# Kernel optimization log

Hardware: AMD Instinct MI355X
Metric: run time of the kernel (lower is better)

The kernel has to match this reference:

```python
import jax, jax.numpy as jnp
import numpy as np

SIG = 512                                   # sigSize
NA = 45                                     # numAngles
SQRT2 = float(np.sqrt(2.0))
DIAG = int(np.ceil(SQRT2 * SIG))            # 725, padded (circle=False) size
PAD = int(np.ceil(SQRT2 * SIG - SIG))       # 213
PAD_BEFORE = (SIG + PAD) // 2 - SIG // 2    # 106
THETA = jnp.asarray(np.deg2rad(np.linspace(0.0, 180.0, NA, endpoint=False)), dtype=jnp.float32)


def _rotate_all(img):
    """Bilinear grid_sample rotation (align_corners=True, zero padding) for all angles.
    img: (B, D, D) -> (B, A, D, D)."""
    D = img.shape[-1]
    c = jnp.linspace(-1.0, 1.0, D, dtype=img.dtype)
    xg = c[None, None, :]                    # column coord j
    yg = c[None, :, None]                    # row coord i
    ct = jnp.cos(THETA)[:, None, None]
    st = jnp.sin(THETA)[:, None, None]
    # affine_grid with R = [[c, s, 0], [-s, c, 0]]
    xs = ct * xg + st * yg                   # (A, D, D)
    ys = -st * xg + ct * yg
    px = (xs + 1.0) * 0.5 * (D - 1)
    py = (ys + 1.0) * 0.5 * (D - 1)
    x0 = jnp.floor(px)
    y0 = jnp.floor(py)
    wx = px - x0
    wy = py - y0
    x0i = x0.astype(jnp.int32)
    y0i = y0.astype(jnp.int32)

    def tap(xi, yi, w):
        valid = (xi >= 0) & (xi < D) & (yi >= 0) & (yi < D)
        xi = jnp.clip(xi, 0, D - 1)
        yi = jnp.clip(yi, 0, D - 1)
        return img[:, yi, xi] * (w * valid)[None]

    return (tap(x0i, y0i, (1 - wx) * (1 - wy)) + tap(x0i + 1, y0i, wx * (1 - wy))
            + tap(x0i, y0i + 1, (1 - wx) * wy) + tap(x0i + 1, y0i + 1, wx * wy))


def radon(x):
    """fmult: x (B,1,S,S) -> sinogram (B,1,D,A), circle=False."""
    xp = jnp.pad(x[:, 0], ((0, 0), (PAD_BEFORE, PAD - PAD_BEFORE), (PAD_BEFORE, PAD - PAD_BEFORE)))
    rot = _rotate_all(xp)                    # (B, A, D, D)
    sino = rot.sum(axis=2)                   # ray-sum over rows -> (B, A, D)
    return jnp.transpose(sino, (0, 2, 1))[:, None]   # (B, 1, D, A)


def iradon(sino):
    """ftran: unfiltered backprojection. sino (B,1,D,A) -> (B,1,S,S)."""
    B, _, D, A = sino.shape
    c = jnp.linspace(-1.0, 1.0, D, dtype=sino.dtype)
    ct = jnp.cos(THETA)[:, None, None]
    st = jnp.sin(THETA)[:, None, None]
    t = ct * c[None, None, :] - st * c[None, :, None]     # (A, D, D) detector coord
    pt = (t + 1.0) * 0.5 * (D - 1)
    t0 = jnp.floor(pt)
    wt = pt - t0
    t0i = t0.astype(jnp.int32)
    s = jnp.transpose(sino[:, 0], (0, 2, 1))               # (B, A, D)

    def tap(ti, w):
        valid = (ti >= 0) & (ti < D)
        tic = jnp.clip(ti, 0, D - 1)
        v = jnp.take_along_axis(s, tic.reshape(1, A, D * D), axis=2).reshape(B, A, D, D)
        return v * (w * valid)[None]

    acc = tap(t0i, 1.0 - wt) + tap(t0i + 1, wt)
    reco = acc.sum(axis=1)                                 # sum over angles
    reco = reco[:, PAD_BEFORE:PAD_BEFORE + SIG, PAD_BEFORE:PAD_BEFORE + SIG]
    return (reco * (jnp.pi / (2.0 * A)))[:, None]


def setup_inputs() -> dict:
    key = jax.random.key(0)
    k1, k2 = jax.random.split(key)
    x = jax.random.normal(k1, (2, 1, SIG, SIG), dtype=jnp.float32)
    y = jax.random.normal(k2, (2, 1, DIAG, NA), dtype=jnp.float32)
    return {"x": x, "y": y}


def reference(x, y):
    # CTClass.grad: per-sample ftran(fmult(x_i) - y_i), vectorized over batch
    return iradon(radon(x) - y)
```

## Files before the change

### kernel.cpp

```cpp
#include <hip/hip_runtime.h>
#include <math.h>

#define SIG 512
#define NA 45
#define DD 725
#define PB 106
#define HALFF 362.0f
#define PI_D 3.14159265358979323846

#define TD2 32
#define TY2 32
#define NT2 23
#define NC42 13
#define RW2 52
#define RH2 47
#define NREG2 640
#define NTILES2 (2 * NA * NT2 * NT2)
#define TGRP (NT2 * NT2)

#define ZSTR 728
#define ZELEMS (2 * NA * ZSTR)
#define TBLOFF ZELEMS
#define DESCOFF 65616
#define DESCI 12
#define BMOFF (DESCOFF + NTILES2 * DESCI)
#define BMWORDS 1492
#define WS_NEED ((BMOFF + BMWORDS) * 4)
#define WS_TBL ((TBLOFF + 2 * NA) * 4)

#define NZB 256
#define NSB 186

#define SEGW2 32

__device__ __forceinline__ float cidx(int i) {
    return -1.0f + (float)i * (2.0f / 724.0f);
}

__device__ __forceinline__ void ref_trig(int a, float& ct, float& st) {
    float thf = (float)((double)(4 * a) * PI_D / 180.0);
    ct = (float)cos((double)thf);
    st = (float)sin((double)thf);
}

__device__ __forceinline__ bool tile_geom(
    int a, int b, int td, int ty, float ct, float st,
    int& dlohi, int& gcb, int& grb, int& nrows, int& kske, int& y0i,
    int& zbase, int& boff, float& pxbase, float& pybase) {
    float X0 = HALFF * (1.0f - ct - st);
    float Y0 = HALFF * (1.0f + st - ct);
    int d0 = td * TD2, dmax = min(d0 + TD2 - 1, DD - 1);
    int y0 = ty * TY2, ymax = min(y0 + TY2 - 1, DD - 1);
    const float lo = (float)(PB - 1), hi = (float)(PB + SIG);

    float Ax0 = fmaf(ct, (float)d0, X0), Ax1 = fmaf(ct, (float)dmax, X0);
    float Axlo = fminf(Ax0, Ax1), Axhi = fmaxf(Ax0, Ax1);
    float Ay0 = fmaf(-st, (float)d0, Y0), Ay1 = fmaf(-st, (float)dmax, Y0);
    float Aylo = fminf(Ay0, Ay1), Ayhi = fmaxf(Ay0, Ay1);
    float ylo = (float)y0, yhi = (float)ymax;
    if (st > 1e-6f) {
        ylo = fmaxf(ylo, (lo - Axhi) / st - 1.0f);
        yhi = fminf(yhi, (hi - Axlo) / st + 1.0f);
    } else if (Axhi <= lo || Axlo >= hi) { return false; }
    if (ct > 1e-6f) {
        ylo = fmaxf(ylo, (lo - Ayhi) / ct - 1.0f);
        yhi = fminf(yhi, (hi - Aylo) / ct + 1.0f);
    } else if (ct < -1e-6f) {
        ylo = fmaxf(ylo, (hi - Aylo) / ct - 1.0f);
        yhi = fminf(yhi, (lo - Ayhi) / ct + 1.0f);
    } else if (Ayhi <= lo || Aylo >= hi) { return false; }
    int yclo = max(y0, (int)ceilf(ylo));
    int ychi = min(ymax, (int)floorf(yhi));
    if (ychi < yclo) return false;
    float yclof = (float)yclo, ychif = (float)ychi;

    float dloF = (float)d0, dhiF = (float)dmax;
    if (ct > 1e-6f) {
        dloF = fmaxf(dloF, (lo - st * ychif - X0) / ct - 1.0f);
        dhiF = fminf(dhiF, (hi - st * yclof - X0) / ct + 1.0f);
    } else if (ct < -1e-6f) {
        dloF = fmaxf(dloF, (hi - st * yclof - X0) / ct - 1.0f);
        dhiF = fminf(dhiF, (lo - st * ychif - X0) / ct + 1.0f);
    }
    if (st > 1e-6f) {
        float yl2 = (ct >= 0.0f) ? yclof : ychif;
        float yh2 = (ct >= 0.0f) ? ychif : yclof;
        dloF = fmaxf(dloF, (Y0 + ct * yl2 - hi) / st - 1.0f);
        dhiF = fminf(dhiF, (Y0 + ct * yh2 - lo) / st + 1.0f);
    }
    int dclo = max(d0, (int)ceilf(dloF));
    int dchi = min(dmax, (int)floorf(dhiF));
    if (dchi < dclo) return false;

    float pxmin = 1e30f, pxmax = -1e30f, pymin = 1e30f, pymax = -1e30f;
    for (int ci = 0; ci < 4; ++ci) {
        float df = (float)((ci & 1) ? dchi : dclo);
        float yf = (float)((ci & 2) ? ychi : yclo);
        float px = fmaf(st, yf, fmaf(ct, df, X0));
        float py = fmaf(ct, yf, fmaf(-st, df, Y0));
        pxmin = fminf(pxmin, px); pxmax = fmaxf(pxmax, px);
        pymin = fminf(pymin, py); pymax = fmaxf(pymax, py);
    }
    int cx0 = (int)floorf(pxmin) - 1;
    int cx1 = (int)floorf(pxmax) + 2;
    int ry0 = (int)floorf(pymin) - 1;
    int ry1 = (int)floorf(pymax) + 2;
    if (cx1 < PB || cx0 >= PB + SIG || ry1 < PB || ry0 >= PB + SIG) return false;

    int cx0a = PB + (((cx0 - PB) >> 2) << 2);
    nrows = min(ry1 - ry0 + 1, RH2);
    gcb = cx0a - PB;
    grb = ry0 - PB;
    dlohi = (dclo - d0) | ((dchi - d0) << 8);
    kske = (yclo - y0) | ((ychi - y0) << 8);
    y0i = y0;
    zbase = (b * NA + a) * ZSTR + 1 + d0;
    boff = b * SIG * SIG;
    pxbase = fmaf(ct, (float)d0, X0) - (float)cx0a;
    pybase = fmaf(-st, (float)d0, Y0) - (float)ry0;
    return true;
}

template <int MODE>
__global__ void prep(const float* __restrict__ yin, float* __restrict__ z,
                     float* __restrict__ tbl, float* __restrict__ zpage,
                     int* __restrict__ desc, unsigned* __restrict__ bmap) {
    __shared__ float s_trig[4];
    __shared__ int s_ag[2];
    if (blockIdx.x < NZB) {
        int i = blockIdx.x * blockDim.x + threadIdx.x;
        if (i < 256) zpage[i] = 0.0f;
        if (MODE >= 1 && blockIdx.x == 0 && threadIdx.x < NA) {
            float ct, st;
            ref_trig(threadIdx.x, ct, st);
            tbl[2 * threadIdx.x] = ct;
            tbl[2 * threadIdx.x + 1] = st;
        }
        if (i >= ZELEMS) return;
        int r = i / ZSTR;
        int c = i - r * ZSTR;
        float v = 0.0f;
        if (c >= 1 && c <= DD) {
            int d = c - 1;
            int a = r % NA;
            int b = r / NA;
            v = -yin[(b * DD + d) * NA + a];
        }
        z[i] = v;
        return;
    }
    if (MODE < 2) return;
    int base = (blockIdx.x - NZB) * blockDim.x;
    if (threadIdx.x < 2) {
        int tl = min(base + (int)threadIdx.x * 255, NTILES2 - 1);
        int ag = tl / TGRP;
        s_ag[threadIdx.x] = ag;
        float ct, st;
        ref_trig(ag % NA, ct, st);
        s_trig[2 * threadIdx.x] = ct;
        s_trig[2 * threadIdx.x + 1] = st;
    }
    __syncthreads();
    int tile = base + threadIdx.x;
    bool live = false;
    int dlohi, gcb, grb, nrows, kske, y0i, zbase, boff;
    float pxbase, pybase;
    float ct = 0.0f, st = 0.0f;
    if (tile < NTILES2) {
        int td = tile % NT2; int rest = tile / NT2;
        int ty = rest % NT2;
        int ag = rest / NT2;
        int a = ag % NA;
        int b = ag / NA;
        int sel = (ag == s_ag[0]) ? 0 : 2;
        ct = s_trig[sel]; st = s_trig[sel + 1];
        live = tile_geom(a, b, td, ty, ct, st, dlohi, gcb, grb, nrows, kske,
                         y0i, zbase, boff, pxbase, pybase);
    }
    unsigned long long m = __ballot(live);
    if ((threadIdx.x & 63) == 0) {
        int w = tile >> 5;
        bmap[w] = (unsigned)m;
        bmap[w + 1] = (unsigned)(m >> 32);
    }
    if (!live) return;
    {
        int nch = (nrows * NC42 + 63) >> 6;
        int rmax = (nch * 64 - 1) / NC42;
        if (grb >= 0 && grb + rmax < SIG && gcb >= 0 && gcb + 52 <= SIG)
            dlohi |= (1 << 16);
    }
    int* dp = desc + tile * DESCI;
    float* fp = (float*)dp;
    dp[0] = dlohi; dp[1] = gcb; dp[2] = grb; dp[3] = nrows;
    dp[4] = kske; fp[5] = pxbase; fp[6] = pybase;
    dp[7] = y0i; dp[8] = zbase; dp[9] = boff;
    fp[10] = ct; fp[11] = st;
}

__device__ __forceinline__ void process_tile32(
    const float* __restrict__ img, const float* __restrict__ zpage,
    float ct, float st,
    int dlohi, int gcb, int grb, int nrows, int kske, int y0i, int zbase,
    float pxbase, float pybase,
    float4* reg4, float* __restrict__ z) {
    float* reg = (float*)reg4;
    int lane = threadIdx.x;

    int nch = (nrows * NC42 + 63) >> 6;
    if (dlohi & (1 << 16)) {
        int r0 = (lane * 5) >> 6;
        int c0 = lane - r0 * NC42;
        const float* src = img + ((grb + r0) << 9) + gcb + (c0 << 2);
        for (int ch = 0; ch < nch; ++ch) {
            __builtin_amdgcn_global_load_lds(
                (const __attribute__((address_space(1))) void*)src,
                (__attribute__((address_space(3))) void*)(reg4 + (ch << 6)),
                16, 0, 0);
            bool cy = (c0 != 0);
            src += cy ? (5 * SIG - 4) : (4 * SIG + 48);
            c0 = cy ? (c0 - 1) : (NC42 - 1);
        }
    } else {
        for (int ch = 0; ch < nch; ++ch) {
            int vi = (ch << 6) + lane;
            int r = vi / NC42;
            int c = vi - r * NC42;
            int gr = grb + r;
            int gc = gcb + (c << 2);
            bool valid = ((unsigned)gr < SIG) & ((unsigned)gc < SIG);
            const float* src = valid ? (img + (gr << 9) + gc) : zpage;
            __builtin_amdgcn_global_load_lds(
                (const __attribute__((address_space(1))) void*)src,
                (__attribute__((address_space(3))) void*)(reg4 + (ch << 6)),
                16, 0, 0);
        }
    }
    __syncthreads();

    int half = lane >> 5;
    int dl = lane & 31;
    int ksb = kske & 255, keb = kske >> 8;
    int dlo = dlohi & 255, dhi = (dlohi >> 8) & 255;
    int n = keb - ksb + 1;
    int sq = ksb + ((n * half) >> 1);
    int eq = ksb + ((n * (half + 1)) >> 1) - 1;

    float lf = (float)min(max(dl, dlo), dhi);
    float pxd = fmaf(ct, lf, pxbase);
    float pyd = fmaf(-st, lf, pybase);
    float yif = (float)(y0i + sq);
    float px = fmaf(st, yif, pxd);
    float py = fmaf(ct, yif, pyd);
    float sum = 0.0f;
#pragma unroll 4
    for (int k = sq; k <= eq; ++k) {
        float fx = floorf(px), fy = floorf(py);
        float wx = px - fx, wy = py - fy;
        int addr = (int)fmaf(fy, (float)RW2, fx);
        float v00 = reg[addr],       v10 = reg[addr + 1];
        float v01 = reg[addr + RW2], v11 = reg[addr + RW2 + 1];
        float top = fmaf(wx, v10 - v00, v00);
        float bot = fmaf(wx, v11 - v01, v01);
        sum = fmaf(wy, bot - top, sum + top);
        px += st; py += ct;
    }
    sum += __shfl_xor(sum, 32);
    if (half == 0 && dl >= dlo && dl <= dhi) {
        atomicAdd(&z[zbase + dl], sum);
    }
}

__global__ __launch_bounds__(64) void radon32f(const float* __restrict__ x,
                                               const float* __restrict__ zpage,
                                               const int* __restrict__ desc,
                                               const unsigned* __restrict__ bmap,
                                               float* __restrict__ z) {
    __shared__ float4 reg4[NREG2];
    unsigned w = bmap[blockIdx.x >> 5];
    if (!((w >> (blockIdx.x & 31)) & 1u)) return;
    const int* dp = desc + blockIdx.x * DESCI;
    const float* fp = (const float*)dp;
    process_tile32(x + dp[9], zpage, fp[10], fp[11],
                   dp[0], dp[1], dp[2], dp[3], dp[4], dp[7], dp[8],
                   fp[5], fp[6], reg4, z);
}

template <int TBL>
__global__ __launch_bounds__(64) void radon32(const float* __restrict__ x,
                                              const float* __restrict__ zpage,
                                              const float* __restrict__ tbl,
                                              float* __restrict__ z) {
    __shared__ float4 reg4[NREG2];
    int tile = blockIdx.x;
    int td = tile % NT2; int rest = tile / NT2;
    int ty = rest % NT2; rest /= NT2;
    int a = rest % NA;
    int b = rest / NA;
    float ct, st;
    if (TBL) { ct = tbl[2 * a]; st = tbl[2 * a + 1]; }
    else     { ref_trig(a, ct, st); }
    int dlohi, gcb, grb, nrows, kske, y0i, zbase, boff;
    float pxbase, pybase;
    if (!tile_geom(a, b, td, ty, ct, st, dlohi, gcb, grb, nrows, kske, y0i,
                   zbase, boff, pxbase, pybase)) return;
    process_tile32(x + boff, zpage, ct, st, dlohi, gcb, grb, nrows, kske,
                   y0i, zbase, pxbase, pybase, reg4, z);
}

template <int TBL>
__global__ __launch_bounds__(256) void iradon16(const float* __restrict__ z,
                                                const float* __restrict__ tbl,
                                                float* __restrict__ out) {
    __shared__ float s_sc[NA], s_st2[NA];
    __shared__ int s_lo[NA];
    __shared__ float s_B[NA * 16];
    __shared__ float s_seg[NA * SEGW2];

    int t = threadIdx.x;
    int b = blockIdx.x >> 10;
    int tb = blockIdx.x & 1023;
    int i0 = (tb >> 5) << 4;
    int j0 = (tb & 31) << 4;

    if (t < NA) {
        float ct, st;
        if (TBL) { ct = tbl[2 * t]; st = tbl[2 * t + 1]; }
        else     { ref_trig(t, ct, st); }
        float sc = ct * HALFF;
        float st2 = -st * HALFF;
        float cxl = cidx(j0 + PB), cxh = cidx(j0 + 15 + PB);
        float cyl = cidx(i0 + PB), cyh = cidx(i0 + 15 + PB);
        float a00 = fmaf(sc, cxl, fmaf(st2, cyl, 363.0f));
        float a01 = fmaf(sc, cxl, fmaf(st2, cyh, 363.0f));
        float a10 = fmaf(sc, cxh, fmaf(st2, cyl, 363.0f));
        float a11 = fmaf(sc, cxh, fmaf(st2, cyh, 363.0f));
        float mn = fminf(fminf(a00, a01), fminf(a10, a11));
        int lo = (int)floorf(mn) - 1;
        lo = min(max(lo, 0), ZSTR - 1 - SEGW2);
        s_sc[t] = sc; s_st2[t] = st2; s_lo[t] = lo;
    }
    __syncthreads();

    for (int s = t; s < NA * 16; s += 256) {
        int a = s >> 4, ii = s & 15;
        s_B[s] = fmaf(s_st2[a], cidx(i0 + ii + PB), 363.0f - (float)s_lo[a]);
    }
    const float* zb = z + b * NA * ZSTR;
    for (int s = t; s < NA * SEGW2; s += 256) {
        int a = s >> 5, idx = s & 31;
        s_seg[s] = zb[a * ZSTR + s_lo[a] + idx];
    }
    __syncthreads();

    float cxv = cidx(j0 + (t & 15) + PB);
    int r0 = t >> 4;
    float acc = 0.f;
    for (int a = 0; a < NA; ++a) {
        float af = fmaf(s_sc[a], cxv, s_B[(a << 4) + r0]);
        float fl = floorf(af);
        float wt = af - fl;
        int ia = (int)fl;
        const float* sp = s_seg + (a << 5) + ia;
        float v0 = sp[0], v1 = sp[1];
        acc = fmaf(wt, v1 - v0, acc + v0);
    }
    const float sfin = (float)(PI_D / (2.0 * NA));
    out[(b << 18) + ((i0 + r0) << 9) + j0 + (t & 15)] = acc * sfin;
}

extern "C" void kernel_launch(void* const* d_in, const int* in_sizes, int n_in,
                              void* d_out, int out_size, void* d_ws, size_t ws_size,
                              hipStream_t stream) {
    const float* x = (const float*)d_in[0];
    const float* yin = (const float*)d_in[1];
    float* out = (float*)d_out;
    float* z = (float*)d_ws;
    float* tbl = z + TBLOFF;
    int* desc = (int*)(z + DESCOFF);
    unsigned* bmap = (unsigned*)(z + BMOFF);
    float* zpage = out;

    if (ws_size >= (size_t)WS_NEED) {
        prep<2><<<NZB + NSB, 256, 0, stream>>>(yin, z, tbl, zpage, desc, bmap);
        radon32f<<<NTILES2, 64, 0, stream>>>(x, zpage, desc, bmap, z);
        iradon16<1><<<2048, 256, 0, stream>>>(z, tbl, out);
    } else if (ws_size >= (size_t)WS_TBL) {
        prep<1><<<NZB, 256, 0, stream>>>(yin, z, tbl, zpage, nullptr, nullptr);
        radon32<1><<<NTILES2, 64, 0, stream>>>(x, zpage, tbl, z);
        iradon16<1><<<2048, 256, 0, stream>>>(z, tbl, out);
    } else {
        prep<0><<<NZB, 256, 0, stream>>>(yin, z, nullptr, zpage, nullptr, nullptr);
        radon32<0><<<NTILES2, 64, 0, stream>>>(x, zpage, nullptr, z);
        iradon16<0><<<2048, 256, 0, stream>>>(z, nullptr, out);
    }
}
```

Baseline: 40.45 us.

## Replace tiled radon with strip blocks writing two half-planes, drop prep and atomics

The radon stage now launches one 64-thread block per (batch, angle, detector column tile, half), looping over 32-row chunks of its half of the ray. Each block writes its partial sums plus half the negated measurement straight into one of two z planes, with no atomics. The backprojection sums the two planes while it loads. This removes the prep kernel, the descriptor/bitmap pass and the atomic adds, cutting three launches to two. In exchange there are far fewer radon blocks (4140 vs ~47k), each looping serially over many rows, which lowers parallelism and may leave long-running blocks.

```diff
diff --git a/kernel.cpp b/kernel.cpp
--- a/kernel.cpp
+++ b/kernel.cpp
@@ -9,28 +9,20 @@
 #define PI_D 3.14159265358979323846
 
 #define TD2 32
-#define TY2 32
 #define NT2 23
 #define NC42 13
 #define RW2 52
 #define RH2 47
 #define NREG2 640
+#define NSTRIP (2 * NA * NT2 * 2)
 #define NTILES2 (2 * NA * NT2 * NT2)
-#define TGRP (NT2 * NT2)
 
 #define ZSTR 728
-#define ZELEMS (2 * NA * ZSTR)
-#define TBLOFF ZELEMS
-#define DESCOFF 65616
-#define DESCI 12
-#define BMOFF (DESCOFF + NTILES2 * DESCI)
-#define BMWORDS 1492
-#define WS_NEED ((BMOFF + BMWORDS) * 4)
-#define WS_TBL ((TBLOFF + 2 * NA) * 4)
+#define ZPLANE (2 * NA * ZSTR)
+#define WS_NEED (2 * ZPLANE * 4)
+#define WS_FB (ZPLANE * 4)
 
 #define NZB 256
-#define NSB 186
-
 #define SEGW2 32
 
 __device__ __forceinline__ float cidx(int i) {
@@ -43,16 +35,266 @@
     st = (float)sin((double)thf);
 }
 
-__device__ __forceinline__ bool tile_geom(
-    int a, int b, int td, int ty, float ct, float st,
-    int& dlohi, int& gcb, int& grb, int& nrows, int& kske, int& y0i,
-    int& zbase, int& boff, float& pxbase, float& pybase) {
+__global__ __launch_bounds__(64) void radon_strip(
+    const float* __restrict__ x, const float* __restrict__ yin,
+    float* __restrict__ z01) {
+    __shared__ float4 reg4[NREG2];
+    float* reg = (float*)reg4;
+    int lane = threadIdx.x;
+
+    int bid = blockIdx.x;
+    int h = bid & 1; bid >>= 1;
+    int td = bid % NT2; bid /= NT2;
+    int a = bid % NA;
+    int b = bid / NA;
+
+    float ct, st;
+    ref_trig(a, ct, st);
     float X0 = HALFF * (1.0f - ct - st);
     float Y0 = HALFF * (1.0f + st - ct);
     int d0 = td * TD2, dmax = min(d0 + TD2 - 1, DD - 1);
-    int y0 = ty * TY2, ymax = min(y0 + TY2 - 1, DD - 1);
     const float lo = (float)(PB - 1), hi = (float)(PB + SIG);
 
+    float Ax0 = fmaf(ct, (float)d0, X0), Ax1 = fmaf(ct, (float)dmax, X0);
+    float Axlo = fminf(Ax0, Ax1), Axhi = fmaxf(Ax0, Ax1);
+    float Ay0 = fmaf(-st, (float)d0, Y0), Ay1 = fmaf(-st, (float)dmax, Y0);
+    float Aylo = fminf(Ay0, Ay1), Ayhi = fmaxf(Ay0, Ay1);
+    float ylo = 0.0f, yhi = (float)(DD - 1);
+    bool dead = false;
+    if (st > 1e-6f) {
+        ylo = fmaxf(ylo, (lo - Axhi) / st - 1.0f);
+        yhi = fminf(yhi, (hi - Axlo) / st + 1.0f);
+    } else if (Axhi <= lo || Axlo >= hi) { dead = true; }
+    if (ct > 1e-6f) {
+        ylo = fmaxf(ylo, (lo - Ayhi) / ct - 1.0f);
+        yhi = fminf(yhi, (hi - Aylo) / ct + 1.0f);
+    } else if (ct < -1e-6f) {
+        ylo = fmaxf(ylo, (hi - Aylo) / ct - 1.0f);
+        yhi = fminf(yhi, (lo - Ayhi) / ct + 1.0f);
+    } else if (Ayhi <= lo || Aylo >= hi) { dead = true; }
+    int yclo = max(0, (int)ceilf(ylo));
+    int ychi = min(DD - 1, (int)floorf(yhi));
+    int hs = 0, he = -1;
+    if (!dead && ychi >= yclo) {
+        int n = ychi - yclo + 1;
+        hs = yclo + ((n * h) >> 1);
+        he = yclo + ((n * (h + 1)) >> 1) - 1;
+    }
+
+    int dl = lane & 31;
+    int half = lane >> 5;
+    int dAbs = d0 + dl;
+    float acc = 0.0f;
+
+    for (int k0 = hs; k0 <= he; k0 += 32) {
+        int k1 = min(k0 + 31, he);
+        float k0f = (float)k0, k1f = (float)k1;
+        float dloF = (float)d0, dhiF = (float)dmax;
+        if (ct > 1e-6f) {
+            dloF = fmaxf(dloF, (lo - st * k1f - X0) / ct - 1.0f);
+            dhiF = fminf(dhiF, (hi - st * k0f - X0) / ct + 1.0f);
+        } else if (ct < -1e-6f) {
+            dloF = fmaxf(dloF, (hi - st * k0f - X0) / ct - 1.0f);
+            dhiF = fminf(dhiF, (lo - st * k1f - X0) / ct + 1.0f);
+        }
+        if (st > 1e-6f) {
+            float yl2 = (ct >= 0.0f) ? k0f : k1f;
+            float yh2 = (ct >= 0.0f) ? k1f : k0f;
+            dloF = fmaxf(dloF, (Y0 + ct * yl2 - hi) / st - 1.0f);
+            dhiF = fminf(dhiF, (Y0 + ct * yh2 - lo) / st + 1.0f);
+        }
+        int dclo = max(d0, (int)ceilf(dloF));
+        int dchi = min(dmax, (int)floorf(dhiF));
+        if (dchi < dclo) continue;
+
+        float pxmin = 1e30f, pxmax = -1e30f, pymin = 1e30f, pymax = -1e30f;
+        for (int ci = 0; ci < 4; ++ci) {
+            float df = (float)((ci & 1) ? dchi : dclo);
+            float yf = (ci & 2) ? k1f : k0f;
+            float px_ = fmaf(st, yf, fmaf(ct, df, X0));
+            float py_ = fmaf(ct, yf, fmaf(-st, df, Y0));
+            pxmin = fminf(pxmin, px_); pxmax = fmaxf(pxmax, px_);
+            pymin = fminf(pymin, py_); pymax = fmaxf(pymax, py_);
+        }
+        int cx0 = (int)floorf(pxmin) - 1;
+        int ry0 = (int)floorf(pymin) - 1;
+        int ry1 = (int)floorf(pymax) + 2;
+        int cx0a = PB + (((cx0 - PB) >> 2) << 2);
+        int gcb = cx0a - PB;
+        int grb = ry0 - PB;
+        int nrows = min(ry1 - ry0 + 1, RH2);
+        int nch = (nrows * NC42 + 63) >> 6;
+
+        __syncthreads();
+
+        if ((grb >= 0) & (grb + 49 < SIG) & (gcb >= 0) & (gcb + 52 <= SIG)) {
+            int r0 = (lane * 5) >> 6;
+            int c0 = lane - r0 * NC42;
+            const float* src = x + (b << 18) + ((grb + r0) << 9) + gcb + (c0 << 2);
+            for (int ch = 0; ch < nch; ++ch) {
+                __builtin_amdgcn_global_load_lds(
+                    (const __attribute__((address_space(1))) void*)src,
+                    (__attribute__((address_space(3))) void*)(reg4 + (ch << 6)),
+                    16, 0, 0);
+                bool cy = (c0 != 0);
+                src += cy ? (5 * SIG - 4) : (4 * SIG + 48);
+                c0 = cy ? (c0 - 1) : (NC42 - 1);
+            }
+        } else {
+            float4 zv = {0.0f, 0.0f, 0.0f, 0.0f};
+            for (int i = lane; i < (nch << 6); i += 64) reg4[i] = zv;
+            asm volatile("s_waitcnt lgkmcnt(0)" ::: "memory");
+            for (int ch = 0; ch < nch; ++ch) {
+                int vi = (ch << 6) + lane;
+                int r = vi / NC42;
+                int c = vi - r * NC42;
+                int gr = grb + r;
+                int gc = gcb + (c << 2);
+                if (((unsigned)gr < SIG) & ((unsigned)gc < SIG)) {
+                    const float* src = x + (b << 18) + (gr << 9) + gc;
+                    __builtin_amdgcn_global_load_lds(
+                        (const __attribute__((address_space(1))) void*)src,
+                        (__attribute__((address_space(3))) void*)(reg4 + (ch << 6)),
+                        16, 0, 0);
+                }
+            }
+        }
+        __syncthreads();
+
+        int wn = k1 - k0 + 1;
+        int sq = k0 + ((wn * half) >> 1);
+        int eq = k0 + ((wn * (half + 1)) >> 1) - 1;
+        float lf = (float)min(max(dAbs, dclo), dchi);
+        float pxb = X0 - (float)cx0a;
+        float pyb = Y0 - (float)ry0;
+        float px = fmaf(st, (float)sq, fmaf(ct, lf, pxb));
+        float py = fmaf(ct, (float)sq, fmaf(-st, lf, pyb));
+        float psum = 0.0f;
+#pragma unroll 4
+        for (int k = sq; k <= eq; ++k) {
+            float fx = floorf(px), fy = floorf(py);
+            float wx = px - fx, wy = py - fy;
+            int addr = (int)fmaf(fy, (float)RW2, fx);
+            float v00 = reg[addr],       v10 = reg[addr + 1];
+            float v01 = reg[addr + RW2], v11 = reg[addr + RW2 + 1];
+            float top = fmaf(wx, v10 - v00, v00);
+            float bot = fmaf(wx, v11 - v01, v01);
+            psum = fmaf(wy, bot - top, psum + top);
+            px += st; py += ct;
+        }
+        acc += (dAbs >= dclo && dAbs <= dchi) ? psum : 0.0f;
+    }
+
+    acc += __shfl_xor(acc, 32);
+    if (half == 0 && dAbs < DD) {
+        float yv = yin[(b * DD + dAbs) * NA + a];
+        z01[h * ZPLANE + (b * NA + a) * ZSTR + 1 + dAbs] =
+            acc - 0.5f * yv;
+    }
+}
+
+template <int TWO>
+__global__ __launch_bounds__(256) void iradon16(const float* __restrict__ z0,
+                                                const float* __restrict__ z1,
+                                                float* __restrict__ out) {
+    __shared__ float s_sc[NA], s_st2[NA];
+    __shared__ int s_lo[NA];
+    __shared__ float s_B[NA * 16];
+    __shared__ float s_seg[NA * SEGW2];
+
+    int t = threadIdx.x;
+    int b = blockIdx.x >> 10;
+    int tb = blockIdx.x & 1023;
+    int i0 = (tb >> 5) << 4;
+    int j0 = (tb & 31) << 4;
+
+    if (t < NA) {
+        float ct, st;
+        ref_trig(t, ct, st);
+        float sc = ct * HALFF;
+        float st2 = -st * HALFF;
+        float cxl = cidx(j0 + PB), cxh = cidx(j0 + 15 + PB);
+        float cyl = cidx(i0 + PB), cyh = cidx(i0 + 15 + PB);
+        float a00 = fmaf(sc, cxl, fmaf(st2, cyl, 363.0f));
+        float a01 = fmaf(sc, cxl, fmaf(st2, cyh, 363.0f));
+        float a10 = fmaf(sc, cxh, fmaf(st2, cyl, 363.0f));
+        float a11 = fmaf(sc, cxh, fmaf(st2, cyh, 363.0f));
+        float mn = fminf(fminf(a00, a01), fminf(a10, a11));
+        int lo = (int)floorf(mn) - 1;
+        lo = min(max(lo, 0), ZSTR - 1 - SEGW2);
+        s_sc[t] = sc; s_st2[t] = st2; s_lo[t] = lo;
+    }
+    __syncthreads();
+
+    for (int s = t; s < NA * 16; s += 256) {
+        int a = s >> 4, ii = s & 15;
+        s_B[s] = fmaf(s_st2[a], cidx(i0 + ii + PB), 363.0f - (float)s_lo[a]);
+    }
+    int zb = b * NA * ZSTR;
+    for (int s = t; s < NA * SEGW2; s += 256) {
+        int a = s >> 5, idx = s & 31;
+        int c = s_lo[a] + idx;
+        float v = 0.0f;
+        if (c >= 1 && c <= DD) {
+            int off = zb + a * ZSTR + c;
+            v = z0[off];
+            if (TWO) v += z1[off];
+        }
+        s_seg[s] = v;
+    }
+    __syncthreads();
+
+    float cxv = cidx(j0 + (t & 15) + PB);
+    int r0 = t >> 4;
+    float acc = 0.f;
+    for (int a = 0; a < NA; ++a) {
+        float af = fmaf(s_sc[a], cxv, s_B[(a << 4) + r0]);
+        float fl = floorf(af);
+        float wt = af - fl;
+        int ia = (int)fl;
+        const float* sp = s_seg + (a << 5) + ia;
+        float v0 = sp[0], v1 = sp[1];
+        acc = fmaf(wt, v1 - v0, acc + v0);
+    }
+    const float sfin = (float)(PI_D / (2.0 * NA));
+    out[(b << 18) + ((i0 + r0) << 9) + j0 + (t & 15)] = acc * sfin;
+}
+
+__global__ void prep_fb(const float* __restrict__ yin, float* __restrict__ z,
+                        float* __restrict__ zpage) {
+    int i = blockIdx.x * blockDim.x + threadIdx.x;
+    if (i < 256) zpage[i] = 0.0f;
+    if (i >= ZPLANE) return;
+    int r = i / ZSTR;
+    int c = i - r * ZSTR;
+    float v = 0.0f;
+    if (c >= 1 && c <= DD) {
+        int d = c - 1;
+        int a = r % NA;
+        int b = r / NA;
+        v = -yin[(b * DD + d) * NA + a];
+    }
+    z[i] = v;
+}
+
+__global__ __launch_bounds__(64) void radon_fb(const float* __restrict__ x,
+                                               const float* __restrict__ zpage,
+                                               float* __restrict__ z) {
+    __shared__ float4 reg4[NREG2];
+    float* reg = (float*)reg4;
+    int lane = threadIdx.x;
+    int tile = blockIdx.x;
+    int td = tile % NT2; int rest = tile / NT2;
+    int ty = rest % NT2; rest /= NT2;
+    int a = rest % NA;
+    int b = rest / NA;
+    float ct, st;
+    ref_trig(a, ct, st);
+    float X0 = HALFF * (1.0f - ct - st);
+    float Y0 = HALFF * (1.0f + st - ct);
+    int d0 = td * TD2, dmax = min(d0 + TD2 - 1, DD - 1);
+    int y0 = ty * TD2, ymax = min(y0 + TD2 - 1, DD - 1);
+    const float lo = (float)(PB - 1), hi = (float)(PB + SIG);
     float Ax0 = fmaf(ct, (float)d0, X0), Ax1 = fmaf(ct, (float)dmax, X0);
     float Axlo = fminf(Ax0, Ax1), Axhi = fmaxf(Ax0, Ax1);
     float Ay0 = fmaf(-st, (float)d0, Y0), Ay1 = fmaf(-st, (float)dmax, Y0);
@@ -61,19 +303,18 @@
     if (st > 1e-6f) {
         ylo = fmaxf(ylo, (lo - Axhi) / st - 1.0f);
         yhi = fminf(yhi, (hi - Axlo) / st + 1.0f);
-    } else if (Axhi <= lo || Axlo >= hi) { return false; }
+    } else if (Axhi <= lo || Axlo >= hi) { return; }
     if (ct > 1e-6f) {
         ylo = fmaxf(ylo, (lo - Ayhi) / ct - 1.0f);
         yhi = fminf(yhi, (hi - Aylo) / ct + 1.0f);
     } else if (ct < -1e-6f) {
         ylo = fmaxf(ylo, (hi - Aylo) / ct - 1.0f);
         yhi = fminf(yhi, (lo - Ayhi) / ct + 1.0f);
-    } else if (Ayhi <= lo || Aylo >= hi) { return false; }
+    } else if (Ayhi <= lo || Aylo >= hi) { return; }
     int yclo = max(y0, (int)ceilf(ylo));
     int ychi = min(ymax, (int)floorf(yhi));
-    if (ychi < yclo) return false;
+    if (ychi < yclo) return;
     float yclof = (float)yclo, ychif = (float)ychi;
-
     float dloF = (float)d0, dhiF = (float)dmax;
     if (ct > 1e-6f) {
         dloF = fmaxf(dloF, (lo - st * ychif - X0) / ct - 1.0f);
@@ -90,8 +331,7 @@
     }
     int dclo = max(d0, (int)ceilf(dloF));
     int dchi = min(dmax, (int)floorf(dhiF));
-    if (dchi < dclo) return false;
-
+    if (dchi < dclo) return;
     float pxmin = 1e30f, pxmax = -1e30f, pymin = 1e30f, pymax = -1e30f;
     for (int ci = 0; ci < 4; ++ci) {
         float df = (float)((ci & 1) ? dchi : dclo);
@@ -102,156 +342,38 @@
         pymin = fminf(pymin, py); pymax = fmaxf(pymax, py);
     }
     int cx0 = (int)floorf(pxmin) - 1;
-    int cx1 = (int)floorf(pxmax) + 2;
     int ry0 = (int)floorf(pymin) - 1;
     int ry1 = (int)floorf(pymax) + 2;
-    if (cx1 < PB || cx0 >= PB + SIG || ry1 < PB || ry0 >= PB + SIG) return false;
-
     int cx0a = PB + (((cx0 - PB) >> 2) << 2);
-    nrows = min(ry1 - ry0 + 1, RH2);
-    gcb = cx0a - PB;
-    grb = ry0 - PB;
-    dlohi = (dclo - d0) | ((dchi - d0) << 8);
-    kske = (yclo - y0) | ((ychi - y0) << 8);
-    y0i = y0;
-    zbase = (b * NA + a) * ZSTR + 1 + d0;
-    boff = b * SIG * SIG;
-    pxbase = fmaf(ct, (float)d0, X0) - (float)cx0a;
-    pybase = fmaf(-st, (float)d0, Y0) - (float)ry0;
-    return true;
-}
-
-template <int MODE>
-__global__ void prep(const float* __restrict__ yin, float* __restrict__ z,
-                     float* __restrict__ tbl, float* __restrict__ zpage,
-                     int* __restrict__ desc, unsigned* __restrict__ bmap) {
-    __shared__ float s_trig[4];
-    __shared__ int s_ag[2];
-    if (blockIdx.x < NZB) {
-        int i = blockIdx.x * blockDim.x + threadIdx.x;
-        if (i < 256) zpage[i] = 0.0f;
-        if (MODE >= 1 && blockIdx.x == 0 && threadIdx.x < NA) {
-            float ct, st;
-            ref_trig(threadIdx.x, ct, st);
-            tbl[2 * threadIdx.x] = ct;
-            tbl[2 * threadIdx.x + 1] = st;
-        }
-        if (i >= ZELEMS) return;
-        int r = i / ZSTR;
-        int c = i - r * ZSTR;
-        float v = 0.0f;
-        if (c >= 1 && c <= DD) {
-            int d = c - 1;
-            int a = r % NA;
-            int b = r / NA;
-            v = -yin[(b * DD + d) * NA + a];
-        }
-        z[i] = v;
-        return;
-    }
-    if (MODE < 2) return;
-    int base = (blockIdx.x - NZB) * blockDim.x;
-    if (threadIdx.x < 2) {
-        int tl = min(base + (int)threadIdx.x * 255, NTILES2 - 1);
-        int ag = tl / TGRP;
-        s_ag[threadIdx.x] = ag;
-        float ct, st;
-        ref_trig(ag % NA, ct, st);
-        s_trig[2 * threadIdx.x] = ct;
-        s_trig[2 * threadIdx.x + 1] = st;
+    int gcb = cx0a - PB;
+    int grb = ry0 - PB;
+    int nrows = min(ry1 - ry0 + 1, RH2);
+    int nch = (nrows * NC42 + 63) >> 6;
+    for (int ch = 0; ch < nch; ++ch) {
+        int vi = (ch << 6) + lane;
+        int r = vi / NC42;
+        int c = vi - r * NC42;
+        int gr = grb + r;
+        int gc = gcb + (c << 2);
+        bool valid = ((unsigned)gr < SIG) & ((unsigned)gc < SIG);
+        const float* src = valid ? (x + (b << 18) + (gr << 9) + gc) : zpage;
+        __builtin_amdgcn_global_load_lds(
+            (const __attribute__((address_space(1))) void*)src,
+            (__attribute__((address_space(3))) void*)(reg4 + (ch << 6)),
+            16, 0, 0);
     }
     __syncthreads();
-    int tile = base + threadIdx.x;
-    bool live = false;
-    int dlohi, gcb, grb, nrows, kske, y0i, zbase, boff;
-    float pxbase, pybase;
-    float ct = 0.0f, st = 0.0f;
-    if (tile < NTILES2) {
-        int td = tile % NT2; int rest = tile / NT2;
-        int ty = rest % NT2;
-        int ag = rest / NT2;
-        int a = ag % NA;
-        int b = ag / NA;
-        int sel = (ag == s_ag[0]) ? 0 : 2;
-        ct = s_trig[sel]; st = s_trig[sel + 1];
-        live = tile_geom(a, b, td, ty, ct, st, dlohi, gcb, grb, nrows, kske,
-                         y0i, zbase, boff, pxbase, pybase);
-    }
-    unsigned long long m = __ballot(live);
-    if ((threadIdx.x & 63) == 0) {
-        int w = tile >> 5;
-        bmap[w] = (unsigned)m;
-        bmap[w + 1] = (unsigned)(m >> 32);
-    }
-    if (!live) return;
-    {
-        int nch = (nrows * NC42 + 63) >> 6;
-        int rmax = (nch * 64 - 1) / NC42;
-        if (grb >= 0 && grb + rmax < SIG && gcb >= 0 && gcb + 52 <= SIG)
-            dlohi |= (1 << 16);
-    }
-    int* dp = desc + tile * DESCI;
-    float* fp = (float*)dp;
-    dp[0] = dlohi; dp[1] = gcb; dp[2] = grb; dp[3] = nrows;
-    dp[4] = kske; fp[5] = pxbase; fp[6] = pybase;
-    dp[7] = y0i; dp[8] = zbase; dp[9] = boff;
-    fp[10] = ct; fp[11] = st;
-}
-
-__device__ __forceinline__ void process_tile32(
-    const float* __restrict__ img, const float* __restrict__ zpage,
-    float ct, float st,
-    int dlohi, int gcb, int grb, int nrows, int kske, int y0i, int zbase,
-    float pxbase, float pybase,
-    float4* reg4, float* __restrict__ z) {
-    float* reg = (float*)reg4;
-    int lane = threadIdx.x;
-
-    int nch = (nrows * NC42 + 63) >> 6;
-    if (dlohi & (1 << 16)) {
-        int r0 = (lane * 5) >> 6;
-        int c0 = lane - r0 * NC42;
-        const float* src = img + ((grb + r0) << 9) + gcb + (c0 << 2);
-        for (int ch = 0; ch < nch; ++ch) {
-            __builtin_amdgcn_global_load_lds(
-                (const __attribute__((address_space(1))) void*)src,
-                (__attribute__((address_space(3))) void*)(reg4 + (ch << 6)),
-                16, 0, 0);
-            bool cy = (c0 != 0);
-            src += cy ? (5 * SIG - 4) : (4 * SIG + 48);
-            c0 = cy ? (c0 - 1) : (NC42 - 1);
-        }
-    } else {
-        for (int ch = 0; ch < nch; ++ch) {
-            int vi = (ch << 6) + lane;
-            int r = vi / NC42;
-            int c = vi - r * NC42;
-            int gr = grb + r;
-            int gc = gcb + (c << 2);
-            bool valid = ((unsigned)gr < SIG) & ((unsigned)gc < SIG);
-            const float* src = valid ? (img + (gr << 9) + gc) : zpage;
-            __builtin_amdgcn_global_load_lds(
-                (const __attribute__((address_space(1))) void*)src,
-                (__attribute__((address_space(3))) void*)(reg4 + (ch << 6)),
-                16, 0, 0);
-        }
-    }
-    __syncthreads();
-
     int half = lane >> 5;
     int dl = lane & 31;
-    int ksb = kske & 255, keb = kske >> 8;
-    int dlo = dlohi & 255, dhi = (dlohi >> 8) & 255;
-    int n = keb - ksb + 1;
-    int sq = ksb + ((n * half) >> 1);
-    int eq = ksb + ((n * (half + 1)) >> 1) - 1;
-
-    float lf = (float)min(max(dl, dlo), dhi);
-    float pxd = fmaf(ct, lf, pxbase);
-    float pyd = fmaf(-st, lf, pybase);
-    float yif = (float)(y0i + sq);
-    float px = fmaf(st, yif, pxd);
-    float py = fmaf(ct, yif, pyd);
+    int n = ychi - yclo + 1;
+    int sq = yclo + ((n * half) >> 1);
+    int eq = yclo + ((n * (half + 1)) >> 1) - 1;
+    int dAbs = d0 + dl;
+    float lf = (float)min(max(dAbs, dclo), dchi);
+    float pxb = X0 - (float)cx0a;
+    float pyb = Y0 - (float)ry0;
+    float px = fmaf(st, (float)sq, fmaf(ct, lf, pxb));
+    float py = fmaf(ct, (float)sq, fmaf(-st, lf, pyb));
     float sum = 0.0f;
 #pragma unroll 4
     for (int k = sq; k <= eq; ++k) {
@@ -266,107 +388,9 @@
         px += st; py += ct;
     }
     sum += __shfl_xor(sum, 32);
-    if (half == 0 && dl >= dlo && dl <= dhi) {
-        atomicAdd(&z[zbase + dl], sum);
-    }
-}
-
-__global__ __launch_bounds__(64) void radon32f(const float* __restrict__ x,
-                                               const float* __restrict__ zpage,
-                                               const int* __restrict__ desc,
-                                               const unsigned* __restrict__ bmap,
-                                               float* __restrict__ z) {
-    __shared__ float4 reg4[NREG2];
-    unsigned w = bmap[blockIdx.x >> 5];
-    if (!((w >> (blockIdx.x & 31)) & 1u)) return;
-    const int* dp = desc + blockIdx.x * DESCI;
-    const float* fp = (const float*)dp;
-    process_tile32(x + dp[9], zpage, fp[10], fp[11],
-                   dp[0], dp[1], dp[2], dp[3], dp[4], dp[7], dp[8],
-                   fp[5], fp[6], reg4, z);
-}
-
-template <int TBL>
-__global__ __launch_bounds__(64) void radon32(const float* __restrict__ x,
-                                              const float* __restrict__ zpage,
-                                              const float* __restrict__ tbl,
-                                              float* __restrict__ z) {
-    __shared__ float4 reg4[NREG2];
-    int tile = blockIdx.x;
-    int td = tile % NT2; int rest = tile / NT2;
-    int ty = rest % NT2; rest /= NT2;
-    int a = rest % NA;
-    int b = rest / NA;
-    float ct, st;
-    if (TBL) { ct = tbl[2 * a]; st = tbl[2 * a + 1]; }
-    else     { ref_trig(a, ct, st); }
-    int dlohi, gcb, grb, nrows, kske, y0i, zbase, boff;
-    float pxbase, pybase;
-    if (!tile_geom(a, b, td, ty, ct, st, dlohi, gcb, grb, nrows, kske, y0i,
-                   zbase, boff, pxbase, pybase)) return;
-    process_tile32(x + boff, zpage, ct, st, dlohi, gcb, grb, nrows, kske,
-                   y0i, zbase, pxbase, pybase, reg4, z);
-}
-
-template <int TBL>
-__global__ __launch_bounds__(256) void iradon16(const float* __restrict__ z,
-                                                const float* __restrict__ tbl,
-                                                float* __restrict__ out) {
-    __shared__ float s_sc[NA], s_st2[NA];
-    __shared__ int s_lo[NA];
-    __shared__ float s_B[NA * 16];
-    __shared__ float s_seg[NA * SEGW2];
-
-    int t = threadIdx.x;
-    int b = blockIdx.x >> 10;
-    int tb = blockIdx.x & 1023;
-    int i0 = (tb >> 5) << 4;
-    int j0 = (tb & 31) << 4;
-
-    if (t < NA) {
-        float ct, st;
-        if (TBL) { ct = tbl[2 * t]; st = tbl[2 * t + 1]; }
-        else     { ref_trig(t, ct, st); }
-        float sc = ct * HALFF;
-        float st2 = -st * HALFF;
-        float cxl = cidx(j0 + PB), cxh = cidx(j0 + 15 + PB);
-        float cyl = cidx(i0 + PB), cyh = cidx(i0 + 15 + PB);
-        float a00 = fmaf(sc, cxl, fmaf(st2, cyl, 363.0f));
-        float a01 = fmaf(sc, cxl, fmaf(st2, cyh, 363.0f));
-        float a10 = fmaf(sc, cxh, fmaf(st2, cyl, 363.0f));
-        float a11 = fmaf(sc, cxh, fmaf(st2, cyh, 363.0f));
-        float mn = fminf(fminf(a00, a01), fminf(a10, a11));
-        int lo = (int)floorf(mn) - 1;
-        lo = min(max(lo, 0), ZSTR - 1 - SEGW2);
-        s_sc[t] = sc; s_st2[t] = st2; s_lo[t] = lo;
-    }
-    __syncthreads();
-
-    for (int s = t; s < NA * 16; s += 256) {
-        int a = s >> 4, ii = s & 15;
-        s_B[s] = fmaf(s_st2[a], cidx(i0 + ii + PB), 363.0f - (float)s_lo[a]);
-    }
-    const float* zb = z + b * NA * ZSTR;
-    for (int s = t; s < NA * SEGW2; s += 256) {
-        int a = s >> 5, idx = s & 31;
-        s_seg[s] = zb[a * ZSTR + s_lo[a] + idx];
-    }
-    __syncthreads();
-
-    float cxv = cidx(j0 + (t & 15) + PB);
-    int r0 = t >> 4;
-    float acc = 0.f;
-    for (int a = 0; a < NA; ++a) {
-        float af = fmaf(s_sc[a], cxv, s_B[(a << 4) + r0]);
-        float fl = floorf(af);
-        float wt = af - fl;
-        int ia = (int)fl;
-        const float* sp = s_seg + (a << 5) + ia;
-        float v0 = sp[0], v1 = sp[1];
-        acc = fmaf(wt, v1 - v0, acc + v0);
-    }
-    const float sfin = (float)(PI_D / (2.0 * NA));
-    out[(b << 18) + ((i0 + r0) << 9) + j0 + (t & 15)] = acc * sfin;
+    if (half == 0 && dAbs >= dclo && dAbs <= dchi) {
+        atomicAdd(&z[(b * NA + a) * ZSTR + 1 + dAbs], sum);
+    }
 }
 
 extern "C" void kernel_launch(void* const* d_in, const int* in_sizes, int n_in,
@@ -375,23 +399,16 @@
     const float* x = (const float*)d_in[0];
     const float* yin = (const float*)d_in[1];
     float* out = (float*)d_out;
-    float* z = (float*)d_ws;
-    float* tbl = z + TBLOFF;
-    int* desc = (int*)(z + DESCOFF);
-    unsigned* bmap = (unsigned*)(z + BMOFF);
-    float* zpage = out;
+    float* z0 = (float*)d_ws;
+    float* z1 = z0 + ZPLANE;
 
     if (ws_size >= (size_t)WS_NEED) {
-        prep<2><<<NZB + NSB, 256, 0, stream>>>(yin, z, tbl, zpage, desc, bmap);
-        radon32f<<<NTILES2, 64, 0, stream>>>(x, zpage, desc, bmap, z);
-        iradon16<1><<<2048, 256, 0, stream>>>(z, tbl, out);
-    } else if (ws_size >= (size_t)WS_TBL) {
-        prep<1><<<NZB, 256, 0, stream>>>(yin, z, tbl, zpage, nullptr, nullptr);
-        radon32<1><<<NTILES2, 64, 0, stream>>>(x, zpage, tbl, z);
-        iradon16<1><<<2048, 256, 0, stream>>>(z, tbl, out);
+        radon_strip<<<NSTRIP, 64, 0, stream>>>(x, yin, z0);
+        iradon16<1><<<2048, 256, 0, stream>>>(z0, z1, out);
     } else {
-        prep<0><<<NZB, 256, 0, stream>>>(yin, z, nullptr, zpage, nullptr, nullptr);
-        radon32<0><<<NTILES2, 64, 0, stream>>>(x, zpage, nullptr, z);
-        iradon16<0><<<2048, 256, 0, stream>>>(z, nullptr, out);
-    }
-}
+        float* zpage = out;
+        prep_fb<<<NZB, 256, 0, stream>>>(yin, z0, zpage);
+        radon_fb<<<NTILES2, 64, 0, stream>>>(x, zpage, z0);
+        iradon16<0><<<2048, 256, 0, stream>>>(z0, z0, out);
+    }
+}
```

Result: slower. 46.75 us (+15.6%).
